# Kernel tuning notes

Measured on AMD Instinct MI355X. Metric: run time of the kernel, lower is better.

The kernel has to match this reference:

```python
import jax, jax.numpy as jnp
import numpy as np

KN = 4        # kernel_number
K = 3         # kernel size
CIN = 256
COUT = 256
BN_EPS = 1e-5


def _rotation_matrices(thetas):
    """thetas: [b, n] -> rot mats [b, n, 9, 9] (faithful port of _get_rotation_matrix)."""
    b, n = thetas.shape
    t = thetas.reshape(-1)                      # [b*n]
    x = jnp.cos(t); y = jnp.sin(t)
    a = x - y; bxy = x * y; c = x + y
    z = jnp.zeros_like(t); o = jnp.ones_like(t)
    pos = [
        [a, 1 - a, z, z, z, z, z, z, z],
        [z, x - bxy, bxy, z, 1 - c + bxy, y - bxy, z, z, z],
        [z, z, a, z, z, 1 - a, z, z, z],
        [bxy, y - bxy, z, x - bxy, 1 - c + bxy, z, z, z, z],
        [z, z, z, z, o, z, z, z, z],
        [z, z, z, z, 1 - c + bxy, x - bxy, z, y - bxy, bxy],
        [z, z, z, 1 - a, z, z, a, z, z],
        [z, z, z, y - bxy, 1 - c + bxy, z, bxy, x - bxy, z],
        [z, z, z, z, z, z, z, 1 - a, a],
    ]
    neg = [
        [c, z, z, 1 - c, z, z, z, z, z],
        [-bxy, x + bxy, z, bxy - y, 1 - a - bxy, z, z, z, z],
        [z, 1 - c, c, z, z, z, z, z, z],
        [z, z, z, x + bxy, 1 - a - bxy, z, -bxy, bxy - y, z],
        [z, z, z, z, o, z, z, z, z],
        [z, bxy - y, -bxy, z, 1 - a - bxy, x + bxy, z, z, z],
        [z, z, z, z, z, z, c, 1 - c, z],
        [z, z, z, z, 1 - a - bxy, bxy - y, z, x + bxy, -bxy],
        [z, z, z, z, z, 1 - c, z, z, c],
    ]
    P = jnp.stack([jnp.stack(r, 0) for r in pos], 0)    # [9, 9, b*n]
    N = jnp.stack([jnp.stack(r, 0) for r in neg], 0)    # [9, 9, b*n]
    R = jnp.where(t >= 0, P, N)                          # [9, 9, b*n]
    return R.transpose(2, 0, 1).reshape(b, n, K * K, K * K)


def _rotate_weights(weights, lambdas, thetas):
    """weights [n, Cout, Cin, 3, 3], lambdas/thetas [b, n] -> [b*Cout, Cin, 3, 3]."""
    b, n = thetas.shape
    _, Cout, Cin, _, _ = weights.shape
    rot = _rotation_matrices(thetas) * lambdas[:, :, None, None]   # [b, n, 9, 9]
    rot = rot.transpose(0, 2, 1, 3).reshape(b * K * K, n * K * K)  # [b*9, n*9]
    w = weights.transpose(0, 3, 4, 1, 2).reshape(n * K * K, Cout * Cin)
    w = rot @ w                                                    # [b*9, Cout*Cin]
    w = w.reshape(b, K, K, Cout, Cin).transpose(0, 3, 4, 1, 2)
    return w.reshape(b * Cout, Cin, K, K)


def _forward(x, weight, w_lambda, w_theta, bn_gamma, bn_beta, bn_mean, bn_var):
    b, Cin, H, W = x.shape
    Cout = weight.shape[1]
    # routing: GAP -> linear heads (sigmoid for lambdas, softsign*pi for thetas)
    pooled = x.mean(axis=(2, 3))                        # [b, Cin]
    lambdas = jax.nn.sigmoid(pooled @ w_lambda)         # [b, n]
    thetas = jax.nn.soft_sign(pooled @ w_theta) * jnp.pi  # [b, n]
    # per-sample rotated weights + grouped conv (groups = b)
    rw = _rotate_weights(weight, lambdas, thetas)       # [b*Cout, Cin, 3, 3]
    xr = x.reshape(1, b * Cin, H, W)
    out = jax.lax.conv_general_dilated(
        xr, rw, window_strides=(1, 1), padding=((1, 1), (1, 1)),
        dimension_numbers=('NCHW', 'OIHW', 'NCHW'), feature_group_count=b)
    out = out.reshape(b, Cout, H, W)
    # BatchNorm (inference, running stats) + ReLU
    inv = jax.lax.rsqrt(bn_var + BN_EPS)
    out = (out - bn_mean[None, :, None, None]) * (inv * bn_gamma)[None, :, None, None] \
          + bn_beta[None, :, None, None]
    return jax.nn.relu(out)


def setup_inputs() -> dict:
    key = jax.random.key(0)
    ks = jax.random.split(key, 8)
    B, H, W = 16, 64, 64
    x = jax.random.normal(ks[0], (B, CIN, H, W), dtype=jnp.float32)
    fan_in = CIN * K * K
    weight = jax.random.normal(ks[1], (KN, COUT, CIN, K, K), dtype=jnp.float32) * np.sqrt(2.0 / fan_in)
    w_lambda = jax.random.normal(ks[2], (CIN, KN), dtype=jnp.float32) * np.sqrt(2.0 / CIN)
    w_theta = jax.random.normal(ks[3], (CIN, KN), dtype=jnp.float32) * np.sqrt(2.0 / CIN)
    bn_gamma = jax.random.uniform(ks[4], (COUT,), dtype=jnp.float32, minval=0.5, maxval=1.5)
    bn_beta = jax.random.normal(ks[5], (COUT,), dtype=jnp.float32) * 0.1
    bn_mean = jax.random.normal(ks[6], (COUT,), dtype=jnp.float32) * 0.1
    bn_var = jax.random.uniform(ks[7], (COUT,), dtype=jnp.float32, minval=0.5, maxval=1.5)
    return {'x': x, 'weight': weight, 'w_lambda': w_lambda, 'w_theta': w_theta,
            'bn_gamma': bn_gamma, 'bn_beta': bn_beta, 'bn_mean': bn_mean, 'bn_var': bn_var}


def reference(x, weight, w_lambda, w_theta, bn_gamma, bn_beta, bn_mean, bn_var):
    return _forward(x, weight, w_lambda, w_theta, bn_gamma, bn_beta, bn_mean, bn_var)
```

## Files before the change

kernel.cpp:

```cpp
#include <hip/hip_runtime.h>
#include <math.h>

typedef __bf16  bf16x8 __attribute__((ext_vector_type(8)));
typedef float   f32x4  __attribute__((ext_vector_type(4)));

#define GLD_LDS16(dst, src)                                                      \
    __builtin_amdgcn_global_load_lds(                                            \
        (const __attribute__((address_space(1))) unsigned int*)(src),            \
        (__attribute__((address_space(3))) unsigned int*)(dst), 16, 0, 0)

__global__ __launch_bounds__(256) void transpose_kernel(const float* __restrict__ x,
                                                        __bf16* __restrict__ xT) {
    int h = blockIdx.x, b = blockIdx.y;
    int lane = threadIdx.x & 63, wv = threadIdx.x >> 6;
#pragma unroll
    for (int i = 0; i < 8; i++) {
        int cq = i * 4 + wv;
        const float* src = x + (((size_t)(b * 256 + cq * 8) * 64 + h) * 64 + lane);
        bf16x8 o;
#pragma unroll
        for (int j = 0; j < 8; j++) o[j] = (__bf16)src[(size_t)j * 4096];
        *(bf16x8*)(xT + (((size_t)(b * 64 + h) * 64 + lane) * 256 + cq * 8)) = o;
    }
}

__global__ __launch_bounds__(256) void pool_kernel(const float* __restrict__ x,
                                                   float* __restrict__ pooled) {
    int bc = blockIdx.x;
    const float* p = x + (size_t)bc * 4096;
    int t = threadIdx.x;
    float s = 0.f;
#pragma unroll
    for (int i = 0; i < 16; i++) s += p[t + i * 256];
#pragma unroll
    for (int off = 32; off > 0; off >>= 1) s += __shfl_down(s, off, 64);
    __shared__ float red[4];
    if ((t & 63) == 0) red[t >> 6] = s;
    __syncthreads();
    if (t == 0) pooled[bc] = (red[0] + red[1] + red[2] + red[3]) * (1.f / 4096.f);
}

__global__ __launch_bounds__(256) void rotw_kernel(
    const float* __restrict__ weight, const float* __restrict__ pooled,
    const float* __restrict__ w_lambda, const float* __restrict__ w_theta,
    __bf16* __restrict__ rwq) {
    __shared__ __attribute__((aligned(16))) float sl[16][4][9][12];
    __shared__ float wlds[4][2304];
    int co = blockIdx.x;
    int t = threadIdx.x;
#pragma unroll
    for (int n = 0; n < 4; n++) {
        const float* wp = weight + ((size_t)n * 256 + co) * 2304;
        for (int i = t; i < 2304; i += 256) wlds[n][i] = wp[i];
    }
    if (t < 64) {
        int b = t >> 2, n = t & 3;
        float zl = 0.f, zt = 0.f;
        for (int ci = 0; ci < 256; ci++) {
            float p = pooled[b * 256 + ci];
            zl += p * w_lambda[ci * 4 + n];
            zt += p * w_theta[ci * 4 + n];
        }
        float lam = 1.f / (1.f + expf(-zl));
        float th  = 3.14159265358979323846f * (zt / (1.f + fabsf(zt)));
        float xc = cosf(th), ys = sinf(th);
        float a = xc - ys, bb = xc * ys, c = xc + ys;
        float R[9][9];
#pragma unroll
        for (int i = 0; i < 9; i++)
#pragma unroll
            for (int j = 0; j < 9; j++) R[i][j] = 0.f;
        if (th >= 0.f) {
            R[0][0] = a;       R[0][1] = 1 - a;
            R[1][1] = xc - bb; R[1][2] = bb;       R[1][4] = 1 - c + bb; R[1][5] = ys - bb;
            R[2][2] = a;       R[2][5] = 1 - a;
            R[3][0] = bb;      R[3][1] = ys - bb;  R[3][3] = xc - bb;    R[3][4] = 1 - c + bb;
            R[4][4] = 1.f;
            R[5][4] = 1 - c + bb; R[5][5] = xc - bb; R[5][7] = ys - bb;  R[5][8] = bb;
            R[6][3] = 1 - a;   R[6][6] = a;
            R[7][3] = ys - bb; R[7][4] = 1 - c + bb; R[7][6] = bb;       R[7][7] = xc - bb;
            R[8][7] = 1 - a;   R[8][8] = a;
        } else {
            R[0][0] = c;       R[0][3] = 1 - c;
            R[1][0] = -bb;     R[1][1] = xc + bb;  R[1][3] = bb - ys;    R[1][4] = 1 - a - bb;
            R[2][1] = 1 - c;   R[2][2] = c;
            R[3][3] = xc + bb; R[3][4] = 1 - a - bb; R[3][6] = -bb;      R[3][7] = bb - ys;
            R[4][4] = 1.f;
            R[5][1] = bb - ys; R[5][2] = -bb;      R[5][4] = 1 - a - bb; R[5][5] = xc + bb;
            R[6][6] = c;       R[6][7] = 1 - c;
            R[7][4] = 1 - a - bb; R[7][5] = bb - ys; R[7][7] = xc + bb;  R[7][8] = -bb;
            R[8][5] = 1 - c;   R[8][8] = c;
        }
#pragma unroll
        for (int p = 0; p < 9; p++) {
#pragma unroll
            for (int q = 0; q < 9; q++) sl[b][n][p][q] = lam * R[p][q];
            sl[b][n][p][9] = sl[b][n][p][10] = sl[b][n][p][11] = 0.f;
        }
    }
    __syncthreads();
    int ci = t;
    float4 wa[4], wb[4];
    float  wc[4];
#pragma unroll
    for (int n = 0; n < 4; n++) {
        const float* wp = &wlds[n][ci * 9];
        wa[n] = make_float4(wp[0], wp[1], wp[2], wp[3]);
        wb[n] = make_float4(wp[4], wp[5], wp[6], wp[7]);
        wc[n] = wp[8];
    }
    for (int b = 0; b < 16; b++) {
#pragma unroll
        for (int p = 0; p < 9; p++) {
            float s = 0.f;
#pragma unroll
            for (int n = 0; n < 4; n++) {
                float4 sa = *(const float4*)&sl[b][n][p][0];
                float4 sb = *(const float4*)&sl[b][n][p][4];
                float  sc = sl[b][n][p][8];
                s += sa.x * wa[n].x + sa.y * wa[n].y + sa.z * wa[n].z + sa.w * wa[n].w
                   + sb.x * wb[n].x + sb.y * wb[n].y + sb.z * wb[n].z + sb.w * wb[n].w
                   + sc * wc[n];
            }
            rwq[(((size_t)b * 9 + p) * 256 + co) * 256 + ci] = (__bf16)s;
        }
    }
}

__global__ __launch_bounds__(256, 2) void conv_kernel(
    const __bf16* __restrict__ xT, const __bf16* __restrict__ rwq,
    const float* __restrict__ bn_gamma, const float* __restrict__ bn_beta,
    const float* __restrict__ bn_mean,  const float* __restrict__ bn_var,
    float* __restrict__ out) {
    __shared__ __attribute__((aligned(16))) __bf16 xs[10][4][66][8];
    __shared__ __attribute__((aligned(16))) __bf16 as9[9][4][66][8];
    __shared__ float bns[64], bnh[64];

    const int t    = threadIdx.x;
    const int lane = t & 63;
    const int wv   = t >> 6;
    const int l15  = lane & 15;
    const int kq4  = lane >> 4;

    const int lin  = blockIdx.x;
    const int r    = lin & 7;
    const int k    = lin >> 3;
    const int b    = (r << 1) | (k >> 5);
    const int inner = k & 31;
    const int co0  = (inner & 3) << 6;
    const int h0   = (inner >> 2) << 3;

    if (t < 64) {
        float inv = rsqrtf(bn_var[co0 + t] + 1e-5f);
        float sc = bn_gamma[co0 + t] * inv;
        bns[t] = sc;
        bnh[t] = bn_beta[co0 + t] - bn_mean[co0 + t] * sc;
    }

    f32x4 acc[2][4][4];
#pragma unroll
    for (int rr = 0; rr < 2; rr++)
#pragma unroll
        for (int m = 0; m < 4; m++)
#pragma unroll
            for (int n = 0; n < 4; n++) acc[rr][m][n] = (f32x4){0.f, 0.f, 0.f, 0.f};

    const uint4 zero4 = {0u, 0u, 0u, 0u};
    if (t < 40) {
        int rr = t >> 2, kq = t & 3;
        *(uint4*)&xs[rr][kq][0][0]  = zero4;
        *(uint4*)&xs[rr][kq][65][0] = zero4;
    }

    for (int ci0 = 0; ci0 < 256; ci0 += 32) {
        __syncthreads();
#pragma unroll
        for (int u = wv * 10; u < wv * 10 + 10; u++) {
            int rr = u >> 2, kq = u & 3;
            int hh = h0 - 1 + rr;
            if (hh >= 0 && hh < 64) {
                const __bf16* src = xT + (((size_t)(b * 64 + hh) * 64 + lane) * 256 + ci0 + kq * 8);
                GLD_LDS16(&xs[rr][kq][1 + lane][0], src);
            } else {
                *(uint4*)&xs[rr][kq][1 + lane][0] = zero4;
            }
        }
#pragma unroll
        for (int u = wv * 9; u < wv * 9 + 9; u++) {
            int tap = u >> 2, kq = u & 3;
            const __bf16* src = rwq +
                ((((size_t)b * 9 + tap) * 256 + co0 + lane) * 256 + ci0 + kq * 8);
            GLD_LDS16(&as9[tap][kq][lane][0], src);
        }
        __syncthreads();
#pragma unroll
        for (int tap = 0; tap < 9; tap++) {
            const int dh = tap / 3, dw = tap % 3;
            bf16x8 af[4];
#pragma unroll
            for (int m = 0; m < 4; m++)
                af[m] = *(const bf16x8*)&as9[tap][kq4][m * 16 + l15][0];
#pragma unroll
            for (int rr = 0; rr < 2; rr++) {
                const int hl = wv + rr * 4;
#pragma unroll
                for (int nt = 0; nt < 4; nt++) {
                    bf16x8 bfr = *(const bf16x8*)&xs[hl + dh][kq4][nt * 16 + l15 + dw][0];
#pragma unroll
                    for (int m = 0; m < 4; m++)
                        acc[rr][m][nt] = __builtin_amdgcn_mfma_f32_16x16x32_bf16(
                            af[m], bfr, acc[rr][m][nt], 0, 0, 0);
                }
            }
        }
    }

#pragma unroll
    for (int rr = 0; rr < 2; rr++) {
        const int h = h0 + wv + rr * 4;
#pragma unroll
        for (int m = 0; m < 4; m++) {
#pragma unroll
            for (int reg = 0; reg < 4; reg++) {
                int col = m * 16 + kq4 * 4 + reg;
                float sc = bns[col], sh = bnh[col];
                int co = co0 + col;
#pragma unroll
                for (int nt = 0; nt < 4; nt++) {
                    int w = nt * 16 + l15;
                    float v = acc[rr][m][nt][reg] * sc + sh;
                    out[(((size_t)b * 256 + co) * 64 + h) * 64 + w] = v > 0.f ? v : 0.f;
                }
            }
        }
    }
}

extern "C" void kernel_launch(void* const* d_in, const int* in_sizes, int n_in,
                              void* d_out, int out_size, void* d_ws, size_t ws_size,
                              hipStream_t stream) {
    const float* x        = (const float*)d_in[0];
    const float* weight   = (const float*)d_in[1];
    const float* w_lambda = (const float*)d_in[2];
    const float* w_theta  = (const float*)d_in[3];
    const float* bn_gamma = (const float*)d_in[4];
    const float* bn_beta  = (const float*)d_in[5];
    const float* bn_mean  = (const float*)d_in[6];
    const float* bn_var   = (const float*)d_in[7];
    float* out = (float*)d_out;

    char* ws = (char*)d_ws;
    float*  pooled  = (float*)(ws);
    __bf16* xT      = (__bf16*)(ws + 49152);
    __bf16* rwq     = (__bf16*)(ws + 49152 + 33554432);

    transpose_kernel<<<dim3(64, 16), 256, 0, stream>>>(x, xT);
    pool_kernel<<<4096, 256, 0, stream>>>(x, pooled);
    rotw_kernel<<<256, 256, 0, stream>>>(weight, pooled, w_lambda, w_theta, rwq);
    conv_kernel<<<512, 256, 0, stream>>>(xT, rwq,
                                         bn_gamma, bn_beta, bn_mean, bn_var, out);
}
```

Baseline: 271.4 us.

## Pool from bf16 transposed input and split rotated-weight kernel across batch groups

The pooling kernel now reads the bf16 channel-last tensor made by the transpose kernel instead of the fp32 input. It runs one block per batch image, with each thread summing one channel over all 4096 pixels, which halves the bytes read. The rotated-weight kernel gains a second grid dimension so each block handles 4 batch images instead of 16. That gives 4x more blocks, at the cost of reloading the weight slice 4 times. The new pooling launch has only 16 blocks, each thread doing a long serial loop, so it may become latency bound, and pooling bf16-rounded values slightly changes numerics.

```diff
diff --git a/kernel.cpp b/kernel.cpp
--- a/kernel.cpp
+++ b/kernel.cpp
@@ -24,37 +24,34 @@
     }
 }
 
-__global__ __launch_bounds__(256) void pool_kernel(const float* __restrict__ x,
+__global__ __launch_bounds__(256) void pool_kernel(const __bf16* __restrict__ xT,
                                                    float* __restrict__ pooled) {
-    int bc = blockIdx.x;
-    const float* p = x + (size_t)bc * 4096;
+    int b = blockIdx.x;
     int t = threadIdx.x;
+    const __bf16* p = xT + (size_t)b * 4096 * 256 + t;
     float s = 0.f;
-#pragma unroll
-    for (int i = 0; i < 16; i++) s += p[t + i * 256];
-#pragma unroll
-    for (int off = 32; off > 0; off >>= 1) s += __shfl_down(s, off, 64);
-    __shared__ float red[4];
-    if ((t & 63) == 0) red[t >> 6] = s;
-    __syncthreads();
-    if (t == 0) pooled[bc] = (red[0] + red[1] + red[2] + red[3]) * (1.f / 4096.f);
+#pragma unroll 8
+    for (int i = 0; i < 4096; i++) s += (float)p[(size_t)i * 256];
+    pooled[b * 256 + t] = s * (1.f / 4096.f);
 }
 
 __global__ __launch_bounds__(256) void rotw_kernel(
     const float* __restrict__ weight, const float* __restrict__ pooled,
     const float* __restrict__ w_lambda, const float* __restrict__ w_theta,
     __bf16* __restrict__ rwq) {
-    __shared__ __attribute__((aligned(16))) float sl[16][4][9][12];
     __shared__ float wlds[4][2304];
+    __shared__ float sl[4][324];
     int co = blockIdx.x;
+    int bg = blockIdx.y * 4;
     int t = threadIdx.x;
 #pragma unroll
     for (int n = 0; n < 4; n++) {
         const float* wp = weight + ((size_t)n * 256 + co) * 2304;
         for (int i = t; i < 2304; i += 256) wlds[n][i] = wp[i];
     }
-    if (t < 64) {
-        int b = t >> 2, n = t & 3;
+    if (t < 16) {
+        int bl = t >> 2, n = t & 3;
+        int b = bg + bl;
         float zl = 0.f, zt = 0.f;
         for (int ci = 0; ci < 256; ci++) {
             float p = pooled[b * 256 + ci];
@@ -92,35 +89,28 @@
             R[8][5] = 1 - c;   R[8][8] = c;
         }
 #pragma unroll
-        for (int p = 0; p < 9; p++) {
-#pragma unroll
-            for (int q = 0; q < 9; q++) sl[b][n][p][q] = lam * R[p][q];
-            sl[b][n][p][9] = sl[b][n][p][10] = sl[b][n][p][11] = 0.f;
-        }
+        for (int p = 0; p < 9; p++)
+#pragma unroll
+            for (int q = 0; q < 9; q++) sl[bl][p * 9 + q + n * 81] = lam * R[p][q];
     }
     __syncthreads();
     int ci = t;
-    float4 wa[4], wb[4];
-    float  wc[4];
-#pragma unroll
-    for (int n = 0; n < 4; n++) {
-        const float* wp = &wlds[n][ci * 9];
-        wa[n] = make_float4(wp[0], wp[1], wp[2], wp[3]);
-        wb[n] = make_float4(wp[4], wp[5], wp[6], wp[7]);
-        wc[n] = wp[8];
-    }
-    for (int b = 0; b < 16; b++) {
+    float w[4][9];
+#pragma unroll
+    for (int n = 0; n < 4; n++)
+#pragma unroll
+        for (int q = 0; q < 9; q++) w[n][q] = wlds[n][ci * 9 + q];
+#pragma unroll
+    for (int bl = 0; bl < 4; bl++) {
+        int b = bg + bl;
 #pragma unroll
         for (int p = 0; p < 9; p++) {
             float s = 0.f;
 #pragma unroll
             for (int n = 0; n < 4; n++) {
-                float4 sa = *(const float4*)&sl[b][n][p][0];
-                float4 sb = *(const float4*)&sl[b][n][p][4];
-                float  sc = sl[b][n][p][8];
-                s += sa.x * wa[n].x + sa.y * wa[n].y + sa.z * wa[n].z + sa.w * wa[n].w
-                   + sb.x * wb[n].x + sb.y * wb[n].y + sb.z * wb[n].z + sb.w * wb[n].w
-                   + sc * wc[n];
+                const float* sp = &sl[bl][n * 81 + p * 9];
+#pragma unroll
+                for (int q = 0; q < 9; q++) s += sp[q] * w[n][q];
             }
             rwq[(((size_t)b * 9 + p) * 256 + co) * 256 + ci] = (__bf16)s;
         }
@@ -255,8 +245,8 @@
     __bf16* rwq     = (__bf16*)(ws + 49152 + 33554432);
 
     transpose_kernel<<<dim3(64, 16), 256, 0, stream>>>(x, xT);
-    pool_kernel<<<4096, 256, 0, stream>>>(x, pooled);
-    rotw_kernel<<<256, 256, 0, stream>>>(weight, pooled, w_lambda, w_theta, rwq);
+    pool_kernel<<<16, 256, 0, stream>>>(xT, pooled);
+    rotw_kernel<<<dim3(256, 4), 256, 0, stream>>>(weight, pooled, w_lambda, w_theta, rwq);
     conv_kernel<<<512, 256, 0, stream>>>(xT, rwq,
                                          bn_gamma, bn_beta, bn_mean, bn_var, out);
 }
```

New measurement: 404.3 us. 1.49x slower.
